# Kernel optimization log

Measured on AMD Instinct MI355X. Metric: run time of the kernel, lower is better.

The kernel has to match this reference:

```python
import jax, jax.numpy as jnp
import numpy as np
from jax.scipy.special import erf, erfc

B, D, C = 256, 512, 85742

def setup_inputs() -> dict:
    key = jax.random.key(0)
    k1, k2, k3, k4, k5 = jax.random.split(key, 5)
    x = jax.random.normal(k1, (B, D), dtype=jnp.float32)
    mu = jax.random.normal(k2, (B, D), dtype=jnp.float32)
    std = jax.random.uniform(k3, (B, D), dtype=jnp.float32)
    weight = jax.random.normal(k4, (C, D), dtype=jnp.float32)
    label = jax.random.randint(k5, (B,), 0, C, dtype=jnp.int64)
    return {"x": x, "mu": mu, "std": std, "weight": weight, "label": label}


def reference(x, mu, std, weight, label):
    # one_hot: [B, C] float, as in F.one_hot(...).float()
    one_hot = jax.nn.one_hot(label, weight.shape[0], dtype=jnp.float32)
    # wy = one_hot @ weight (embedding gather expressed as GEMM), wi = (1 - one_hot) @ weight
    wy = one_hot @ weight                 # [B, D]
    wi = (1.0 - one_hot) @ weight         # [B, D]
    sqrt2 = jnp.sqrt(jnp.float32(2.0))
    # torch.dist(a, b) is the scalar Frobenius (L2) distance
    dist_y = jnp.abs(jnp.sqrt(jnp.sum((wy - mu) ** 2)))
    dist_i = jnp.abs(jnp.sqrt(jnp.sum((wi - mu) ** 2)))
    erf_value = erf(dist_y / (sqrt2 * std))    # [B, D] via broadcast of scalar dist
    erfc_value = erfc(dist_i / (sqrt2 * std))  # [B, D]
    loss = erf_value.sum() + erfc_value.sum()
    return loss
```

## Files before the change

kernel.cpp:

```cpp
#include <hip/hip_runtime.h>
#include <math.h>

#define DDIM 512
#define BDIM 256
#define NCLS 85742
#define NB1 2048
#define CHUNK1 ((NCLS + NB1 - 1) / NB1)

typedef float f32x4 __attribute__((ext_vector_type(4)));

__device__ __forceinline__ float wave_reduce(float v) {
    #pragma unroll
    for (int off = 32; off > 0; off >>= 1)
        v += __shfl_down(v, off, 64);
    return v;
}

__device__ __forceinline__ float block_reduce(float v, float* smem) {
    const int lane = threadIdx.x & 63;
    const int wid  = threadIdx.x >> 6;
    v = wave_reduce(v);
    if (lane == 0) smem[wid] = v;
    __syncthreads();
    if (wid == 0) {
        v = (lane < (int)(blockDim.x >> 6)) ? smem[lane] : 0.0f;
        v = wave_reduce(v);
    }
    return v;
}

#define WS_UPART 1024
#define WS_PART  (1024 + 256 * 128 * 4)

__global__ __launch_bounds__(256, 4)
void colsum_partial(const float* __restrict__ W, const float* __restrict__ mu,
                    const int* __restrict__ label, float* __restrict__ ws,
                    float* __restrict__ out) {
    const int t = threadIdx.x;
    const int b = blockIdx.x;
    if (b == 0 && t < 2) {
        if (t == 0) { ws[0] = 0.0f; *out = 0.0f; }
    }
    const int q = t & 127;
    const int rsub = t >> 7;
    const f32x4* __restrict__ W4 = reinterpret_cast<const f32x4*>(W) + q;

    const int r0 = b * CHUNK1;
    const int r1 = (r0 + CHUNK1 < NCLS) ? (r0 + CHUNK1) : NCLS;

    f32x4 a0 = (f32x4)(0.f), a1 = a0, a2 = a0, a3 = a0;

    if (r1 - r0 == CHUNK1) {
        const f32x4* base = W4 + (size_t)(r0 + rsub) * 128;
        f32x4 c0 = base[0];
        f32x4 c1 = base[256];
        f32x4 c2 = base[512];
        f32x4 c3 = base[768];
        #pragma unroll
        for (int k = 1; k <= 4; ++k) {
            const f32x4* p = base + (size_t)k * 1024;
            a0 += c0;  c0 = p[0];
            a1 += c1;  c1 = p[256];
            a2 += c2;  c2 = p[512];
            a3 += c3;  c3 = p[768];
        }
        f32x4 cl = base[5120];
        a0 += c0; a1 += c1; a2 += c2; a3 += c3;
        a0 += cl;
    } else {
        for (int r = r0 + rsub; r < r1; r += 2)
            a0 += W4[(size_t)r * 128];
    }
    a0 += a1 + a2 + a3;

    __shared__ f32x4 smem[128];
    if (rsub) smem[q] = a0;
    __syncthreads();
    if (!rsub) {
        a0 += smem[q];
        f32x4* partialT = reinterpret_cast<f32x4*>(ws + WS_PART);
        partialT[(size_t)q * NB1 + b] = a0;
    }

    if (b < 128) {
        const int row = 2 * b + rsub;
        const int lab = label[row];
        const f32x4 m4 = reinterpret_cast<const f32x4*>(mu)[(size_t)row * 128 + q];
        const f32x4 w4 = reinterpret_cast<const f32x4*>(W)[(size_t)lab * 128 + q];
        f32x4 d = w4 - m4;
        f32x4 u = w4 + m4;
        reinterpret_cast<f32x4*>(ws + WS_UPART)[(size_t)row * 128 + q] = u;
        float syp = d.x * d.x + d.y * d.y + d.z * d.z + d.w * d.w;
        float s2p = u.x * u.x + u.y * u.y + u.z * u.z + u.w * u.w;
        __shared__ float rsm[8];
        __syncthreads();
        syp = block_reduce(syp, rsm);
        __syncthreads();
        s2p = block_reduce(s2p, rsm);
        if (t == 0) {
            ws[16 + b]  = syp;
            ws[144 + b] = s2p;
        }
    }
}

__global__ __launch_bounds__(256, 4)
void reduce_kernel(float* __restrict__ ws) {
    const int q = blockIdx.x;
    const int t = threadIdx.x;
    const f32x4* __restrict__ partialT =
        reinterpret_cast<const f32x4*>(ws + WS_PART) + (size_t)q * NB1;
    f32x4 s = (f32x4)(0.f);
    #pragma unroll
    for (int k = 0; k < NB1 / 256; ++k)
        s += partialT[t + k * 256];
    f32x4 u = reinterpret_cast<const f32x4*>(ws + WS_UPART)[(size_t)t * 128 + q];

    float sx = wave_reduce(s.x), sy = wave_reduce(s.y);
    float sz = wave_reduce(s.z), sw = wave_reduce(s.w);
    float ux = wave_reduce(u.x), uy = wave_reduce(u.y);
    float uz = wave_reduce(u.z), uw = wave_reduce(u.w);
    __shared__ f32x4 sm[4], um[4];
    if ((t & 63) == 0) {
        sm[t >> 6] = (f32x4)(sx, sy, sz, sw);
        um[t >> 6] = (f32x4)(ux, uy, uz, uw);
    }
    __syncthreads();
    if (t == 0) {
        f32x4 cs = (sm[0] + sm[1]) + (sm[2] + sm[3]);
        f32x4 U  = (um[0] + um[1]) + (um[2] + um[3]);
        f32x4 si4 = 256.0f * cs * cs - 2.0f * cs * U;
        atomicAdd(&ws[0], si4.x + si4.y + si4.z + si4.w);
    }

    if (q == 0) {
        __syncthreads();
        __shared__ float rsm[8];
        float syp = (t < 128) ? ws[16 + t]  : 0.0f;
        float s2p = (t < 128) ? ws[144 + t] : 0.0f;
        syp = block_reduce(syp, rsm);
        __syncthreads();
        s2p = block_reduce(s2p, rsm);
        if (t == 0) { ws[1] = syp; ws[2] = s2p; }
    }
}

__global__ __launch_bounds__(256, 4)
void loss_kernel(const float* __restrict__ stdv, const float* __restrict__ ws,
                 float* __restrict__ out) {
    __shared__ float smem[8];
    const float dy = sqrtf(ws[1]);
    const float di = sqrtf(ws[0] + ws[2]);
    const float inv_sqrt2 = 0.70710678118654752f;
    const int i = blockIdx.x * 256 + threadIdx.x;
    f32x4 s4 = reinterpret_cast<const f32x4*>(stdv)[i];
    float acc;
    {
        float rx = inv_sqrt2 / s4.x, ry = inv_sqrt2 / s4.y;
        float rz = inv_sqrt2 / s4.z, rw = inv_sqrt2 / s4.w;
        acc  = erff(dy * rx) + erfcf(di * rx);
        acc += erff(dy * ry) + erfcf(di * ry);
        acc += erff(dy * rz) + erfcf(di * rz);
        acc += erff(dy * rw) + erfcf(di * rw);
    }
    acc = block_reduce(acc, smem);
    if (threadIdx.x == 0) atomicAdd(out, acc);
}

extern "C" void kernel_launch(void* const* d_in, const int* in_sizes, int n_in,
                              void* d_out, int out_size, void* d_ws, size_t ws_size,
                              hipStream_t stream) {
    const float* mu    = (const float*)d_in[1];
    const float* stdv  = (const float*)d_in[2];
    const float* W     = (const float*)d_in[3];
    const int*   label = (const int*)d_in[4];
    float* out = (float*)d_out;
    float* ws  = (float*)d_ws;

    colsum_partial<<<NB1, 256, 0, stream>>>(W, mu, label, ws, out);
    reduce_kernel<<<128, 256, 0, stream>>>(ws);
    loss_kernel<<<128, 256, 0, stream>>>(stdv, ws, out);
}
```

Before: 43.43 us.

## Fuse reduce and loss kernels using a global atomic counter barrier

```diff
diff --git a/kernel.cpp b/kernel.cpp
--- a/kernel.cpp
+++ b/kernel.cpp
@@ -8,6 +8,9 @@
 #define CHUNK1 ((NCLS + NB1 - 1) / NB1)
 
 typedef float f32x4 __attribute__((ext_vector_type(4)));
+
+#define WS_UPART 1024
+#define WS_PART  (1024 + 256 * 128 * 4)
 
 __device__ __forceinline__ float wave_reduce(float v) {
     #pragma unroll
@@ -29,17 +32,15 @@
     return v;
 }
 
-#define WS_UPART 1024
-#define WS_PART  (1024 + 256 * 128 * 4)
-
 __global__ __launch_bounds__(256, 4)
 void colsum_partial(const float* __restrict__ W, const float* __restrict__ mu,
                     const int* __restrict__ label, float* __restrict__ ws,
                     float* __restrict__ out) {
     const int t = threadIdx.x;
     const int b = blockIdx.x;
-    if (b == 0 && t < 2) {
-        if (t == 0) { ws[0] = 0.0f; *out = 0.0f; }
+    if (b == 0 && t == 0) {
+        ws[0] = 0.0f; *out = 0.0f;
+        *reinterpret_cast<unsigned int*>(ws + 8) = 0u;
     }
     const int q = t & 127;
     const int rsub = t >> 7;
@@ -105,7 +106,8 @@
 }
 
 __global__ __launch_bounds__(256, 4)
-void reduce_kernel(float* __restrict__ ws) {
+void reduce_loss(float* __restrict__ ws, const float* __restrict__ stdv,
+                 float* __restrict__ out) {
     const int q = blockIdx.x;
     const int t = threadIdx.x;
     const f32x4* __restrict__ partialT =
@@ -143,17 +145,25 @@
         s2p = block_reduce(s2p, rsm);
         if (t == 0) { ws[1] = syp; ws[2] = s2p; }
     }
-}
 
-__global__ __launch_bounds__(256, 4)
-void loss_kernel(const float* __restrict__ stdv, const float* __restrict__ ws,
-                 float* __restrict__ out) {
-    __shared__ float smem[8];
-    const float dy = sqrtf(ws[1]);
-    const float di = sqrtf(ws[0] + ws[2]);
+    __syncthreads();
+    __shared__ float sc[3];
+    unsigned int* cnt = reinterpret_cast<unsigned int*>(ws + 8);
+    if (t == 0) {
+        __threadfence();
+        atomicAdd(cnt, 1u);
+        while (__hip_atomic_load(cnt, __ATOMIC_ACQUIRE,
+                                 __HIP_MEMORY_SCOPE_AGENT) < 128u) {}
+        sc[0] = __hip_atomic_load(&ws[0], __ATOMIC_RELAXED, __HIP_MEMORY_SCOPE_AGENT);
+        sc[1] = __hip_atomic_load(&ws[1], __ATOMIC_RELAXED, __HIP_MEMORY_SCOPE_AGENT);
+        sc[2] = __hip_atomic_load(&ws[2], __ATOMIC_RELAXED, __HIP_MEMORY_SCOPE_AGENT);
+    }
+    __syncthreads();
+
+    const float dy = sqrtf(sc[1]);
+    const float di = sqrtf(sc[0] + sc[2]);
     const float inv_sqrt2 = 0.70710678118654752f;
-    const int i = blockIdx.x * 256 + threadIdx.x;
-    f32x4 s4 = reinterpret_cast<const f32x4*>(stdv)[i];
+    f32x4 s4 = reinterpret_cast<const f32x4*>(stdv)[q * 256 + t];
     float acc;
     {
         float rx = inv_sqrt2 / s4.x, ry = inv_sqrt2 / s4.y;
@@ -163,8 +173,9 @@
         acc += erff(dy * rz) + erfcf(di * rz);
         acc += erff(dy * rw) + erfcf(di * rw);
     }
-    acc = block_reduce(acc, smem);
-    if (threadIdx.x == 0) atomicAdd(out, acc);
+    __shared__ float lsm[8];
+    acc = block_reduce(acc, lsm);
+    if (t == 0) atomicAdd(out, acc);
 }
 
 extern "C" void kernel_launch(void* const* d_in, const int* in_sizes, int n_in,
@@ -178,6 +189,5 @@
     float* ws  = (float*)d_ws;
 
     colsum_partial<<<NB1, 256, 0, stream>>>(W, mu, label, ws, out);
-    reduce_kernel<<<128, 256, 0, stream>>>(ws);
-    loss_kernel<<<128, 256, 0, stream>>>(stdv, ws, out);
+    reduce_loss<<<128, 256, 0, stream>>>(ws, stdv, out);
 }
```

Measured after the change: 46.02 us. +6.0%, slower.
